# Kernel tuning notes

Hardware: AMD Instinct MI355X
Metric: run time of the kernel (lower is better)

The kernel has to match this reference:

```python
import math
import jax, jax.numpy as jnp
import numpy as np


def _scharr(img):
    # img: (..., H, W) -> (..., 2, H, W); F.conv2d is cross-correlation, as is lax.conv
    kx = jnp.array([[-3., 0., 3.], [10., 0., 10.], [-3., 0., 3.]], jnp.float32)
    k = jnp.stack([kx, kx.T])[:, None]  # (2,1,3,3)
    lead = img.shape[:-2]
    x = img.reshape((-1, 1) + img.shape[-2:])
    y = jax.lax.conv_general_dilated(x, k, (1, 1), 'SAME',
                                     dimension_numbers=('NCHW', 'OIHW', 'NCHW'))
    return y.reshape(lead + (2,) + img.shape[-2:])


def _rotate_nearest(x, angle_deg):
    # torchvision-style rotate with expand=True, nearest interpolation, zero fill
    H, W = x.shape[-2], x.shape[-1]
    a = math.radians(angle_deg)
    c, s = math.cos(a), math.sin(a)
    Hn = int(math.ceil(abs(W * s) + abs(H * c)))
    Wn = int(math.ceil(abs(W * c) + abs(H * s)))
    yy, xx = jnp.meshgrid(jnp.arange(Hn, dtype=jnp.float32),
                          jnp.arange(Wn, dtype=jnp.float32), indexing='ij')
    xg = xx - (Wn - 1) / 2.0
    yg = yy - (Hn - 1) / 2.0
    xi = c * xg - s * yg + (W - 1) / 2.0
    yi = s * xg + c * yg + (H - 1) / 2.0
    xn = jnp.round(xi).astype(jnp.int32)
    yn = jnp.round(yi).astype(jnp.int32)
    valid = (xn >= 0) & (xn < W) & (yn >= 0) & (yn < H)
    out = x[..., jnp.clip(yn, 0, H - 1), jnp.clip(xn, 0, W - 1)]
    return jnp.where(valid, out, jnp.zeros((), x.dtype))


def _gauss_derivs(img):
    # image_gaussian_derivatives: (B, C, H, W) -> (B, C, 8, H, W)
    H, W = img.shape[-2:]
    g = _scharr(img)  # (B, C, 2, H, W)
    # rotated_xywh(H, W, 45) to get crop offsets, exactly as in the source
    a = math.radians(45.0)
    al, be = math.cos(a), math.sin(a)
    cx, cy = W / 2.0, H / 2.0
    pts = [(0., 0.), (W - 1., 0.), (0., H - 1.), (W - 1., H - 1.)]
    rx = [al * px + be * py + (1 - al) * cx - be * cy for px, py in pts]
    ry = [-be * px + al * py + be * cx + (1 - al) * cy for px, py in pts]
    w45 = max(rx) - min(rx)
    h45 = max(ry) - min(ry)
    startx = int(max(0, (w45 - W) / 2))
    starty = int(max(0, (h45 - H) / 2))
    gr = _scharr(_rotate_nearest(img, 45.0))      # (B, C, 2, Hr, Wr)
    grb = _rotate_nearest(gr, -45.0)
    grc = grb[..., starty:starty + H, startx:startx + W]  # (B, C, 2, H, W)
    return jnp.concatenate([jnp.clip(g, 0, None), jnp.clip(g, None, 0),
                            jnp.clip(grc, 0, None), jnp.clip(grc, None, 0)], axis=-3)


def _normalize_min_max(x):
    hmin = x.min(axis=(-2, -1), keepdims=True)
    hmax = x.max(axis=(-2, -1), keepdims=True)
    return (x - hmin) / (hmax - hmin)


def _batched_hist(Z, nbins):
    # Z: (..., N) int in [0, nbins) -> per-row histogram (..., nbins) via one fused segment_sum
    lead = Z.shape[:-1]
    L = int(np.prod(lead))
    Zf = Z.reshape(L, -1)
    ids = (jnp.arange(L, dtype=jnp.int32)[:, None] * nbins + Zf).ravel()
    h = jax.ops.segment_sum(jnp.ones(ids.shape, jnp.float32), ids, num_segments=L * nbins)
    return h.reshape(lead + (nbins,))


def setup_inputs() -> dict:
    key = jax.random.key(0)
    k1, k2 = jax.random.split(key)
    img = jax.random.uniform(k1, (2, 3, 512, 512), jnp.float32)
    reg_lab = jax.random.randint(k2, (2, 1, 3, 512, 512), 0, 256, dtype=jnp.int32)
    return {'img': img, 'reg_lab': reg_lab,
            'color_bins': 25, 'texture_bins': 10, 'num_segments': 256}


def reference(img, reg_lab, color_bins, texture_bins, num_segments):
    B, I, G, H, W = reg_lab.shape
    C = img.shape[1]
    S = num_segments
    # normalized oriented gradient features (B, C, 8, H, W)
    tex = _normalize_min_max(_gauss_derivs(img))
    # region sizes: scatter_add of ones over region labels
    region_sizes = _batched_hist(reg_lab.reshape(B, I, G, H * W), S)  # (B,I,G,S)
    # color histograms
    Zc = (reg_lab[:, :, :, None].astype(jnp.float32) * color_bins
          + img[:, None, None] * (color_bins - 1)).astype(jnp.int32)  # (B,I,G,C,H,W)
    ch = _batched_hist(Zc.reshape(B, I, G, C, H * W), S * color_bins)
    ch = jnp.moveaxis(ch.reshape(B, I, G, C, S, color_bins), -2, -3)  # (B,I,G,S,C,cb)
    ch = ch / ch.sum(axis=(-2, -1), keepdims=True)
    # texture histograms
    Zt = (reg_lab[:, :, :, None, None].astype(jnp.float32) * texture_bins
          + tex[:, None, None] * (texture_bins - 1)).astype(jnp.int32)  # (B,I,G,C,8,H,W)
    th = _batched_hist(Zt.reshape(B, I, G, C, 8, H * W), S * texture_bins)
    th = jnp.moveaxis(th.reshape(B, I, G, C, 8, S, texture_bins), -2, -4)  # (B,I,G,S,C,8,tb)
    th = th / th.sum(axis=(-3, -2, -1), keepdims=True)
    # per-region bounding boxes via segment min/max (replaces the 5-deep python loop)
    grid_y, grid_x = jnp.meshgrid(jnp.arange(H, dtype=jnp.int32),
                                  jnp.arange(W, dtype=jnp.int32), indexing='ij')
    BIG = B * I * G
    ids = (jnp.arange(BIG, dtype=jnp.int32)[:, None] * S
           + reg_lab.reshape(BIG, H * W)).ravel()
    xs = jnp.tile(grid_x.ravel(), BIG)
    ys = jnp.tile(grid_y.ravel(), BIG)
    n = BIG * S
    xmin = jax.ops.segment_min(xs, ids, num_segments=n)
    xmax = jax.ops.segment_max(xs, ids, num_segments=n)
    ymin = jax.ops.segment_min(ys, ids, num_segments=n)
    ymax = jax.ops.segment_max(ys, ids, num_segments=n)
    nonempty = region_sizes.reshape(n) > 0
    xmin = jnp.where(nonempty, xmin, W)
    ymin = jnp.where(nonempty, ymin, H)
    xmax = jnp.where(nonempty, xmax, 0)
    ymax = jnp.where(nonempty, ymax, 0)
    xywh = jnp.stack([xmin, ymin, xmax - xmin, ymax - ymin], axis=-1).reshape(B, I, G, S, 4)
    return region_sizes, ch, th, xywh
```

## Files before the change

### kernel.cpp

```cpp
#include <hip/hip_runtime.h>
#include <climits>

#define HW 262144
#define IW 512
#define RN 725
#define NSEG 256
#define CH_OFF 1536
#define TH_OFF 116736
#define XY_OFF 485376
#define NBLK 256
#define THP 24
#define CHP 32

#define ASTR 67
#define RSTR 73
#define ROFF 156

static __device__ __forceinline__ float rtap_l(const float* __restrict__ Rt,
                                               int rx0, int ry0, int cx, int cy) {
    if (cx < 0 || cx >= RN || cy < 0 || cy >= RN) return 0.f;
    const float cs = 0.7071067811865476f;
    float xg = (float)cx - 362.0f;
    float yg = (float)cy - 362.0f;
    float xi = cs * xg - cs * yg + 255.5f;
    float yi = cs * xg + cs * yg + 255.5f;
    int xs = (int)rintf(xi);
    int ys = (int)rintf(yi);
    if (xs < 0 || xs >= IW || ys < 0 || ys >= IW) return 0.f;
    return Rt[(ys - ry0) * RSTR + (xs - rx0)];
}

static __device__ __forceinline__ void mm_of_map(const float* __restrict__ pmin,
                                                 const float* __restrict__ pmax,
                                                 int m, float* slo, float* shi,
                                                 float& mn, float& mx) {
    int tid = threadIdx.x;
    float lo = 3.4e38f, hi = -3.4e38f;
    for (int i = tid; i < NBLK; i += 256) {
        lo = fminf(lo, pmin[m * NBLK + i]);
        hi = fmaxf(hi, pmax[m * NBLK + i]);
    }
    slo[tid] = lo; shi[tid] = hi;
    __syncthreads();
    for (int off = 128; off > 0; off >>= 1) {
        if (tid < off) {
            slo[tid] = fminf(slo[tid], slo[tid + off]);
            shi[tid] = fmaxf(shi[tid], shi[tid + off]);
        }
        __syncthreads();
    }
    mn = slo[0]; mx = shi[0];
    __syncthreads();
}

__global__ __launch_bounds__(256) void k_grad(
    const float* __restrict__ img, const int* __restrict__ lab,
    float* __restrict__ gmaps,
    float* __restrict__ pmin, float* __restrict__ pmax,
    float* __restrict__ out, int* __restrict__ bbmin, int* __restrict__ bbmax,
    unsigned char* __restrict__ lab8)
{
    int t = blockIdx.x;
    int bc = blockIdx.y;
    int tid = threadIdx.x;
    if (bc == 0 && t < 6) {
        out[t * 256 + tid] = 0.0f;
    } else if (bc == 1 && t < 12) {
        int i = t * 256 + tid;
        bbmin[i] = INT_MAX;
        bbmax[i] = INT_MIN;
    }
    {
        int i = t * 256 + tid;
        int4 l = ((const int4*)(lab + (size_t)bc * HW))[i];
        unsigned v = (unsigned)(l.x & 255) | ((unsigned)(l.y & 255) << 8) |
                     ((unsigned)(l.z & 255) << 16) | ((unsigned)(l.w & 255) << 24);
        ((unsigned*)(lab8 + (size_t)bc * HW))[i] = v;
    }
    __shared__ float At[18 * ASTR];
    __shared__ float Rt[24 * RSTR];
    __shared__ float slo[4][256], shi[4][256];
    int tx0 = (t & 7) << 6;
    int ty0 = (t >> 3) << 4;
    const float* im = img + (size_t)bc * HW;
    int lane = tid & 63, wr = tid >> 6;
    for (int r = wr; r < 18; r += 4) {
        int gy = ty0 - 1 + r;
        bool yok = (gy >= 0 && gy < IW);
        int gx = tx0 - 1 + lane;
        At[r * ASTR + lane] = (yok && gx >= 0 && gx < IW) ? im[gy * IW + gx] : 0.f;
        if (lane < 2) {
            int gx2 = gx + 64;
            At[r * ASTR + lane + 64] = (yok && gx2 >= 0 && gx2 < IW) ? im[gy * IW + gx2] : 0.f;
        }
    }
    for (int r = wr; r < 24; r += 4) {
        int gy = ty0 - ROFF + r;
        bool yok = (gy >= 0 && gy < IW);
        int gx = tx0 - ROFF + lane;
        Rt[r * RSTR + lane] = (yok && gx >= 0 && gx < IW) ? im[gy * IW + gx] : 0.f;
        if (lane < 8) {
            int gx2 = gx + 64;
            Rt[r * RSTR + lane + 64] = (yok && gx2 >= 0 && gx2 < IW) ? im[gy * IW + gx2] : 0.f;
        }
    }
    __syncthreads();
    const float cs = 0.7071067811865476f;
    int rx0 = tx0 - ROFF, ry0 = ty0 - ROFF;
    float mn0 = 3.4e38f, mx0 = -3.4e38f, mn1 = 3.4e38f, mx1 = -3.4e38f;
    float mn2 = 3.4e38f, mx2 = -3.4e38f, mn3 = 3.4e38f, mx3 = -3.4e38f;
    #pragma unroll
    for (int it = 0; it < 4; ++it) {
        int ly = wr * 4 + it;
        int x = tx0 + lane, y = ty0 + ly;
        int p = y * IW + x;
        const float* Ar = At + ly * ASTR + lane;
        float a  = Ar[0],            b2 = Ar[1],            c2 = Ar[2];
        float d2 = Ar[ASTR],                                 e2 = Ar[ASTR + 2];
        float f2 = Ar[2 * ASTR],     h2 = Ar[2 * ASTR + 1], i9 = Ar[2 * ASTR + 2];
        float g0 = -3.f*a + 3.f*c2 + 10.f*d2 + 10.f*e2 - 3.f*f2 + 3.f*i9;
        float g1 = -3.f*a + 10.f*b2 - 3.f*c2 + 3.f*f2 + 10.f*h2 + 3.f*i9;
        gmaps[((size_t)(bc*2+0))*HW + p] = g0;
        gmaps[((size_t)(bc*2+1))*HW + p] = g1;
        float xgc = (float)(x + 105) - 512.5f;
        float ygc = (float)(y + 105) - 512.5f;
        float t1 = cs * xgc, t2 = cs * ygc;
        float xi = (t1 + t2) + 362.0f;
        float yi = (-t1 + t2) + 362.0f;
        int xn = (int)rintf(xi);
        int yn = (int)rintf(yi);
        float r0 = 0.f, r1 = 0.f;
        if (xn >= 0 && xn < RN && yn >= 0 && yn < RN) {
            float ra = rtap_l(Rt, rx0, ry0, xn-1, yn-1);
            float rb = rtap_l(Rt, rx0, ry0, xn,   yn-1);
            float rc = rtap_l(Rt, rx0, ry0, xn+1, yn-1);
            float rd = rtap_l(Rt, rx0, ry0, xn-1, yn);
            float re = rtap_l(Rt, rx0, ry0, xn+1, yn);
            float rf = rtap_l(Rt, rx0, ry0, xn-1, yn+1);
            float rh = rtap_l(Rt, rx0, ry0, xn,   yn+1);
            float ri = rtap_l(Rt, rx0, ry0, xn+1, yn+1);
            r0 = -3.f*ra + 3.f*rc + 10.f*rd + 10.f*re - 3.f*rf + 3.f*ri;
            r1 = -3.f*ra + 10.f*rb - 3.f*rc + 3.f*rf + 10.f*rh + 3.f*ri;
        }
        gmaps[((size_t)(12 + bc*2+0))*HW + p] = r0;
        gmaps[((size_t)(12 + bc*2+1))*HW + p] = r1;
        mn0 = fminf(mn0, g0); mx0 = fmaxf(mx0, g0);
        mn1 = fminf(mn1, g1); mx1 = fmaxf(mx1, g1);
        mn2 = fminf(mn2, r0); mx2 = fmaxf(mx2, r0);
        mn3 = fminf(mn3, r1); mx3 = fmaxf(mx3, r1);
    }
    slo[0][tid] = mn0; shi[0][tid] = mx0;
    slo[1][tid] = mn1; shi[1][tid] = mx1;
    slo[2][tid] = mn2; shi[2][tid] = mx2;
    slo[3][tid] = mn3; shi[3][tid] = mx3;
    __syncthreads();
    for (int off = 128; off > 0; off >>= 1) {
        if (tid < off) {
            #pragma unroll
            for (int k = 0; k < 4; ++k) {
                slo[k][tid] = fminf(slo[k][tid], slo[k][tid + off]);
                shi[k][tid] = fmaxf(shi[k][tid], shi[k][tid + off]);
            }
        }
        __syncthreads();
    }
    if (tid < 4) {
        int m = (tid < 2) ? (bc*2 + tid) : (12 + bc*2 + (tid - 2));
        pmin[m * NBLK + t] = slo[tid][0];
        pmax[m * NBLK + t] = shi[tid][0];
    }
}

__global__ __launch_bounds__(256) void k_regchist(
    const float* __restrict__ img, const unsigned char* __restrict__ lab8,
    float* __restrict__ rs_out, int* __restrict__ bbmin, int* __restrict__ bbmax,
    unsigned* __restrict__ chp)
{
    __shared__ unsigned cnt[NSEG * 25];
    __shared__ unsigned rcnt[NSEG];
    __shared__ int sxmin[NSEG], sxmax[NSEG], symin[NSEG], symax[NSEG];
    int gy = blockIdx.y;
    int c = gy % 3;
    int bg = gy / 3;
    int b = bg / 3;
    int tid = threadIdx.x;
    bool do_reg = (c == 0);
    for (int i = tid; i < NSEG * 25; i += 256) cnt[i] = 0;
    if (do_reg) {
        rcnt[tid] = 0; sxmin[tid] = INT_MAX; sxmax[tid] = INT_MIN;
        symin[tid] = INT_MAX; symax[tid] = INT_MIN;
    }
    __syncthreads();
    const float4* ip = (const float4*)(img + ((size_t)b * 3 + c) * HW);
    const unsigned* lp = (const unsigned*)(lab8 + (size_t)bg * HW);
    int stride = 256 * gridDim.x;
    for (int i = blockIdx.x * 256 + tid; i < HW / 4; i += stride) {
        float4 v4 = ip[i];
        unsigned l4 = lp[i];
        int l0 = l4 & 255, l1 = (l4 >> 8) & 255, l2 = (l4 >> 16) & 255, l3 = l4 >> 24;
        int b0 = (int)((float)l0 * 25.0f + v4.x * 24.0f);
        int b1 = (int)((float)l1 * 25.0f + v4.y * 24.0f);
        int b2 = (int)((float)l2 * 25.0f + v4.z * 24.0f);
        int b3 = (int)((float)l3 * 25.0f + v4.w * 24.0f);
        b0 = min(max(b0, 0), 6399); b1 = min(max(b1, 0), 6399);
        b2 = min(max(b2, 0), 6399); b3 = min(max(b3, 0), 6399);
        atomicAdd(&cnt[b0], 1u); atomicAdd(&cnt[b1], 1u);
        atomicAdd(&cnt[b2], 1u); atomicAdd(&cnt[b3], 1u);
        if (do_reg) {
            int p = i << 2;
            int y = p >> 9, x = p & 511;
            atomicAdd(&rcnt[l0], 1u); atomicAdd(&rcnt[l1], 1u);
            atomicAdd(&rcnt[l2], 1u); atomicAdd(&rcnt[l3], 1u);
            atomicMin(&sxmin[l0], x);     atomicMax(&sxmax[l0], x);
            atomicMin(&sxmin[l1], x + 1); atomicMax(&sxmax[l1], x + 1);
            atomicMin(&sxmin[l2], x + 2); atomicMax(&sxmax[l2], x + 2);
            atomicMin(&sxmin[l3], x + 3); atomicMax(&sxmax[l3], x + 3);
            atomicMin(&symin[l0], y); atomicMax(&symax[l0], y);
            atomicMin(&symin[l1], y); atomicMax(&symax[l1], y);
            atomicMin(&symin[l2], y); atomicMax(&symax[l2], y);
            atomicMin(&symin[l3], y); atomicMax(&symax[l3], y);
        }
    }
    __syncthreads();
    unsigned* dst = chp + ((size_t)gy * CHP + blockIdx.x) * 6400;
    for (int i = tid; i < NSEG * 25; i += 256) dst[i] = cnt[i];
    if (do_reg) {
        if (rcnt[tid]) atomicAdd(&rs_out[bg * NSEG + tid], (float)rcnt[tid]);
        if (sxmin[tid] != INT_MAX) {
            atomicMin(&bbmin[bg * NSEG + tid], sxmin[tid]);
            atomicMax(&bbmax[bg * NSEG + tid], sxmax[tid]);
            atomicMin(&bbmin[1536 + bg * NSEG + tid], symin[tid]);
            atomicMax(&bbmax[1536 + bg * NSEG + tid], symax[tid]);
        }
    }
}

__global__ __launch_bounds__(256) void k_thist(
    const float* __restrict__ maps, const unsigned char* __restrict__ lab8,
    const float* __restrict__ pmin, const float* __restrict__ pmax,
    unsigned* __restrict__ thp)
{
    __shared__ unsigned cnt[5120];
    __shared__ float slo[256], shi[256];
    int gy = blockIdx.y;
    int split = blockIdx.x;
    int gi = gy % 3;
    int r = gy / 3;
    int base = r & 1;
    int bd = r >> 1;
    int d = bd & 1;
    int bc = bd >> 1;
    int b = bc / 3;
    int m = base * 12 + bc * 2 + d;
    float mn, mx;
    mm_of_map(pmin, pmax, m, slo, shi, mn, mx);
    for (int i = threadIdx.x; i < 5120; i += 256) cnt[i] = 0;
    __syncthreads();
    float hminp = fmaxf(mn, 0.f), denp = fmaxf(mx, 0.f) - hminp;
    float hminn = fminf(mn, 0.f), denn = fminf(mx, 0.f) - hminn;
    const float4* src = (const float4*)(maps + (size_t)m * HW);
    const unsigned* lp = (const unsigned*)(lab8 + (size_t)(b * 3 + gi) * HW);
    for (int i = split * 256 + threadIdx.x; i < HW / 4; i += 256 * THP) {
        float4 v4 = src[i];
        unsigned l4 = lp[i];
#define TH1(V, SH)                                                     \
        {                                                              \
            float v = (V);                                             \
            bool ge = (v >= 0.f);                                      \
            float hm = ge ? hminp : hminn;                             \
            float dn = ge ? denp : denn;                               \
            float t9 = ((v - hm) / dn) * 9.0f;                         \
            int bi = (int)((float)((l4 >> SH) & 255u) * 10.0f + t9);   \
            bi = min(max(bi, 0), 2559);                                \
            atomicAdd(&cnt[(ge ? 0 : 2560) + bi], 1u);                 \
        }
        TH1(v4.x, 0) TH1(v4.y, 8) TH1(v4.z, 16) TH1(v4.w, 24)
#undef TH1
    }
    __syncthreads();
    unsigned* dst = thp + ((size_t)(gy * THP + split)) * 5120;
    for (int i = threadIdx.x; i < 5120; i += 256) dst[i] = cnt[i];
}

__global__ __launch_bounds__(256) void k_thfinal(
    const unsigned* __restrict__ thp, const unsigned* __restrict__ chp,
    const float* __restrict__ pmin, const float* __restrict__ pmax,
    const int* __restrict__ bbmin, const int* __restrict__ bbmax,
    float* __restrict__ out)
{
    int tid = threadIdx.x;
    int bx = blockIdx.x;
    if (bx < 288) {
        __shared__ unsigned hist[1280];
        __shared__ float slo[256], shi[256];
        int gy = bx >> 2;
        int ck = bx & 3;
        int l0 = ck << 6;
        int gi = gy % 3; int r = gy / 3; int base = r & 1;
        int bd = r >> 1; int d = bd & 1; int bc = bd >> 1;
        int b = bc / 3, c = bc - b * 3;
        int m = base * 12 + bc * 2 + d;
        float mn, mx;
        mm_of_map(pmin, pmax, m, slo, shi, mn, mx);
        int g0off = l0 * 10;
        for (int i = tid; i < 1280; i += 256) {
            int g = (i < 640) ? (g0off + i) : (2560 + g0off + (i - 640));
            unsigned s = 0;
            #pragma unroll 4
            for (int p = 0; p < THP; ++p) s += thp[((size_t)(gy * THP + p)) * 5120 + g];
            hist[i] = s;
        }
        __syncthreads();
        if (tid < 64) {
            int l = l0 + tid;
            unsigned nge = 0;
            for (int tb = 0; tb < 10; ++tb) nge += hist[tid * 10 + tb];
            float rsf = out[(b * 3 + gi) * NSEG + l];
            unsigned rsu = (unsigned)rsf;
            unsigned nlt = (rsu >= nge) ? (rsu - nge) : 0u;
            float hminp = fmaxf(mn, 0.f), denp = fmaxf(mx, 0.f) - hminp;
            float hminn = fminf(mn, 0.f), denn = fminf(mx, 0.f) - hminn;
            float la = (float)l;
            float tp0 = ((0.0f - hminp) / denp) * 9.0f;
            float tn0 = ((0.0f - hminn) / denn) * 9.0f;
            int bp = (int)(la * 10.0f + tp0); bp = min(max(bp, 0), 2559);
            int bn = (int)(la * 10.0f + tn0); bn = min(max(bn, 0), 2559);
            if (nlt && bp >= g0off && bp < g0off + 640) atomicAdd(&hist[bp - g0off], nlt);
            if (nge && bn >= g0off && bn < g0off + 640) atomicAdd(&hist[640 + bn - g0off], nge);
        }
        __syncthreads();
        for (int i = tid; i < 1280; i += 256) {
            int pos = (i < 640);
            int rr = pos ? i : i - 640;
            int seg = l0 + rr / 10, tb = rr % 10;
            int tt = base * 4 + (pos ? 0 : 2) + d;
            float rsf = out[(b * 3 + gi) * NSEG + seg];
            out[TH_OFF + ((size_t)((b * 3 + gi) * NSEG + seg) * 3 + c) * 80 + tt * 10 + tb] =
                (float)hist[i] / (24.0f * rsf);
        }
    } else {
        for (int seg = bx - 288; seg < 1536; seg += (gridDim.x - 288)) {
            int bg = seg >> 8;
            int s = seg & 255;
            float rsf = out[seg];
            float cd = 3.0f * rsf;
            float* ch = out + CH_OFF + (size_t)seg * 75;
            for (int i = tid; i < 75; i += 256) {
                int c = i / 25, cb = i - c * 25;
                unsigned sum = 0;
                const unsigned* src = chp + ((size_t)(bg * 3 + c) * CHP) * 6400 + s * 25 + cb;
                #pragma unroll 4
                for (int p = 0; p < CHP; ++p) sum += src[(size_t)p * 6400];
                ch[i] = (float)sum / cd;
            }
            if (tid == 0) {
                int xmin, xmax, ymin, ymax;
                if (rsf > 0.f) {
                    xmin = bbmin[seg]; ymin = bbmin[1536 + seg];
                    xmax = bbmax[seg]; ymax = bbmax[1536 + seg];
                } else {
                    xmin = IW; ymin = IW; xmax = 0; ymax = 0;
                }
                float* xy = out + XY_OFF + (size_t)seg * 4;
                xy[0] = (float)xmin; xy[1] = (float)ymin;
                xy[2] = (float)(xmax - xmin); xy[3] = (float)(ymax - ymin);
            }
        }
    }
}

extern "C" void kernel_launch(void* const* d_in, const int* in_sizes, int n_in,
                              void* d_out, int out_size, void* d_ws, size_t ws_size,
                              hipStream_t stream) {
    const float* img = (const float*)d_in[0];
    const int* lab = (const int*)d_in[1];
    float* out = (float*)d_out;

    float* gmaps = (float*)d_ws;
    float* pmin = gmaps + (size_t)24 * HW;
    float* pmax = pmin + 24 * NBLK;
    int* bbmin = (int*)(pmax + 24 * NBLK);
    int* bbmax = bbmin + 3072;
    unsigned* thp = (unsigned*)(bbmax + 3072);
    unsigned* chp = thp + (size_t)72 * THP * 5120;
    unsigned char* lab8 = (unsigned char*)(chp + (size_t)18 * CHP * 6400);

    hipLaunchKernelGGL(k_grad, dim3(NBLK, 6), dim3(256), 0, stream,
                       img, lab, gmaps, pmin, pmax, out, bbmin, bbmax, lab8);
    hipLaunchKernelGGL(k_regchist, dim3(CHP, 18), dim3(256), 0, stream,
                       img, lab8, out, bbmin, bbmax, chp);
    hipLaunchKernelGGL(k_thist, dim3(THP, 72), dim3(256), 0, stream, gmaps, lab8, pmin, pmax, thp);
    hipLaunchKernelGGL(k_thfinal, dim3(288 + 256), dim3(256), 0, stream, thp, chp, pmin, pmax, bbmin, bbmax, out);
}
```

Baseline: 131.8 us.

## Merge color and texture histogram kernels into one interleaved launch with packed 16-bit counters

Fuses k_regchist and k_thist into a single k_hist launch, giving every fourth block the color/region work and the other three the texture work, so the two histogram workloads run concurrently. The goal is to drop one launch and fill the GPU better. Color and region counts are now packed as two 16-bit counters per 32-bit word in shared memory, roughly halving the shared footprint to allow more resident blocks. The finalize kernel is widened to one block per segment instead of a strided loop. The packed counters risk overflow if a bin exceeds 65535 within a block's slice, but each slice holds only 8192 pixels, so they stay in range.

```diff
diff --git a/kernel.cpp b/kernel.cpp
--- a/kernel.cpp
+++ b/kernel.cpp
@@ -171,115 +171,128 @@
     }
 }
 
-__global__ __launch_bounds__(256) void k_regchist(
-    const float* __restrict__ img, const unsigned char* __restrict__ lab8,
-    float* __restrict__ rs_out, int* __restrict__ bbmin, int* __restrict__ bbmax,
-    unsigned* __restrict__ chp)
+__global__ __launch_bounds__(256) void k_hist(
+    const float* __restrict__ maps, const float* __restrict__ img,
+    const unsigned char* __restrict__ lab8,
+    const float* __restrict__ pmin, const float* __restrict__ pmax,
+    unsigned* __restrict__ thp, unsigned* __restrict__ chp,
+    float* __restrict__ rs_out, int* __restrict__ bbmin, int* __restrict__ bbmax)
 {
-    __shared__ unsigned cnt[NSEG * 25];
-    __shared__ unsigned rcnt[NSEG];
-    __shared__ int sxmin[NSEG], sxmax[NSEG], symin[NSEG], symax[NSEG];
-    int gy = blockIdx.y;
-    int c = gy % 3;
-    int bg = gy / 3;
-    int b = bg / 3;
+    __shared__ __align__(16) unsigned char smem[23040];
+    int bxid = blockIdx.x;
     int tid = threadIdx.x;
-    bool do_reg = (c == 0);
-    for (int i = tid; i < NSEG * 25; i += 256) cnt[i] = 0;
-    if (do_reg) {
-        rcnt[tid] = 0; sxmin[tid] = INT_MAX; sxmax[tid] = INT_MIN;
-        symin[tid] = INT_MAX; symax[tid] = INT_MIN;
-    }
-    __syncthreads();
-    const float4* ip = (const float4*)(img + ((size_t)b * 3 + c) * HW);
-    const unsigned* lp = (const unsigned*)(lab8 + (size_t)bg * HW);
-    int stride = 256 * gridDim.x;
-    for (int i = blockIdx.x * 256 + tid; i < HW / 4; i += stride) {
-        float4 v4 = ip[i];
-        unsigned l4 = lp[i];
-        int l0 = l4 & 255, l1 = (l4 >> 8) & 255, l2 = (l4 >> 16) & 255, l3 = l4 >> 24;
-        int b0 = (int)((float)l0 * 25.0f + v4.x * 24.0f);
-        int b1 = (int)((float)l1 * 25.0f + v4.y * 24.0f);
-        int b2 = (int)((float)l2 * 25.0f + v4.z * 24.0f);
-        int b3 = (int)((float)l3 * 25.0f + v4.w * 24.0f);
-        b0 = min(max(b0, 0), 6399); b1 = min(max(b1, 0), 6399);
-        b2 = min(max(b2, 0), 6399); b3 = min(max(b3, 0), 6399);
-        atomicAdd(&cnt[b0], 1u); atomicAdd(&cnt[b1], 1u);
-        atomicAdd(&cnt[b2], 1u); atomicAdd(&cnt[b3], 1u);
+    if ((bxid & 3) != 3) {
+        int idx = bxid - (bxid >> 2);
+        int gy = idx / THP;
+        int split = idx - gy * THP;
+        unsigned* cnt = (unsigned*)smem;
+        float* slo = (float*)(smem + 20480);
+        float* shi = slo + 256;
+        int gi = gy % 3;
+        int r = gy / 3;
+        int base = r & 1;
+        int bd = r >> 1;
+        int d = bd & 1;
+        int bc = bd >> 1;
+        int b = bc / 3;
+        int m = base * 12 + bc * 2 + d;
+        float mn, mx;
+        mm_of_map(pmin, pmax, m, slo, shi, mn, mx);
+        for (int i = tid; i < 5120; i += 256) cnt[i] = 0;
+        __syncthreads();
+        float hminp = fmaxf(mn, 0.f), denp = fmaxf(mx, 0.f) - hminp;
+        float hminn = fminf(mn, 0.f), denn = fminf(mx, 0.f) - hminn;
+        const float4* src = (const float4*)(maps + (size_t)m * HW);
+        const unsigned* lp = (const unsigned*)(lab8 + (size_t)(b * 3 + gi) * HW);
+        for (int i = split * 256 + tid; i < HW / 4; i += 256 * THP) {
+            float4 v4 = src[i];
+            unsigned l4 = lp[i];
+#define TH1(V, SH)                                                     \
+            {                                                          \
+                float v = (V);                                         \
+                bool ge = (v >= 0.f);                                  \
+                float hm = ge ? hminp : hminn;                         \
+                float dn = ge ? denp : denn;                           \
+                float t9 = ((v - hm) / dn) * 9.0f;                     \
+                int bi = (int)((float)((l4 >> SH) & 255u) * 10.0f + t9); \
+                bi = min(max(bi, 0), 2559);                            \
+                atomicAdd(&cnt[(ge ? 0 : 2560) + bi], 1u);             \
+            }
+            TH1(v4.x, 0) TH1(v4.y, 8) TH1(v4.z, 16) TH1(v4.w, 24)
+#undef TH1
+        }
+        __syncthreads();
+        unsigned* dst = thp + ((size_t)(gy * THP + split)) * 5120;
+        for (int i = tid; i < 5120; i += 256) dst[i] = cnt[i];
+    } else {
+        int w = bxid >> 2;
+        int gy = w >> 5;
+        int sp = w & 31;
+        int c = gy % 3;
+        int bg = gy / 3;
+        int b = bg / 3;
+        unsigned* pk = (unsigned*)smem;
+        unsigned* prc = pk + 3200;
+        int* sxmin = (int*)(prc + 128);
+        int* sxmax = sxmin + NSEG;
+        int* symin = sxmax + NSEG;
+        int* symax = symin + NSEG;
+        bool do_reg = (c == 0);
+        for (int i = tid; i < 3200; i += 256) pk[i] = 0;
         if (do_reg) {
-            int p = i << 2;
-            int y = p >> 9, x = p & 511;
-            atomicAdd(&rcnt[l0], 1u); atomicAdd(&rcnt[l1], 1u);
-            atomicAdd(&rcnt[l2], 1u); atomicAdd(&rcnt[l3], 1u);
-            atomicMin(&sxmin[l0], x);     atomicMax(&sxmax[l0], x);
-            atomicMin(&sxmin[l1], x + 1); atomicMax(&sxmax[l1], x + 1);
-            atomicMin(&sxmin[l2], x + 2); atomicMax(&sxmax[l2], x + 2);
-            atomicMin(&sxmin[l3], x + 3); atomicMax(&sxmax[l3], x + 3);
-            atomicMin(&symin[l0], y); atomicMax(&symax[l0], y);
-            atomicMin(&symin[l1], y); atomicMax(&symax[l1], y);
-            atomicMin(&symin[l2], y); atomicMax(&symax[l2], y);
-            atomicMin(&symin[l3], y); atomicMax(&symax[l3], y);
-        }
-    }
-    __syncthreads();
-    unsigned* dst = chp + ((size_t)gy * CHP + blockIdx.x) * 6400;
-    for (int i = tid; i < NSEG * 25; i += 256) dst[i] = cnt[i];
-    if (do_reg) {
-        if (rcnt[tid]) atomicAdd(&rs_out[bg * NSEG + tid], (float)rcnt[tid]);
-        if (sxmin[tid] != INT_MAX) {
-            atomicMin(&bbmin[bg * NSEG + tid], sxmin[tid]);
-            atomicMax(&bbmax[bg * NSEG + tid], sxmax[tid]);
-            atomicMin(&bbmin[1536 + bg * NSEG + tid], symin[tid]);
-            atomicMax(&bbmax[1536 + bg * NSEG + tid], symax[tid]);
-        }
-    }
-}
-
-__global__ __launch_bounds__(256) void k_thist(
-    const float* __restrict__ maps, const unsigned char* __restrict__ lab8,
-    const float* __restrict__ pmin, const float* __restrict__ pmax,
-    unsigned* __restrict__ thp)
-{
-    __shared__ unsigned cnt[5120];
-    __shared__ float slo[256], shi[256];
-    int gy = blockIdx.y;
-    int split = blockIdx.x;
-    int gi = gy % 3;
-    int r = gy / 3;
-    int base = r & 1;
-    int bd = r >> 1;
-    int d = bd & 1;
-    int bc = bd >> 1;
-    int b = bc / 3;
-    int m = base * 12 + bc * 2 + d;
-    float mn, mx;
-    mm_of_map(pmin, pmax, m, slo, shi, mn, mx);
-    for (int i = threadIdx.x; i < 5120; i += 256) cnt[i] = 0;
-    __syncthreads();
-    float hminp = fmaxf(mn, 0.f), denp = fmaxf(mx, 0.f) - hminp;
-    float hminn = fminf(mn, 0.f), denn = fminf(mx, 0.f) - hminn;
-    const float4* src = (const float4*)(maps + (size_t)m * HW);
-    const unsigned* lp = (const unsigned*)(lab8 + (size_t)(b * 3 + gi) * HW);
-    for (int i = split * 256 + threadIdx.x; i < HW / 4; i += 256 * THP) {
-        float4 v4 = src[i];
-        unsigned l4 = lp[i];
-#define TH1(V, SH)                                                     \
-        {                                                              \
-            float v = (V);                                             \
-            bool ge = (v >= 0.f);                                      \
-            float hm = ge ? hminp : hminn;                             \
-            float dn = ge ? denp : denn;                               \
-            float t9 = ((v - hm) / dn) * 9.0f;                         \
-            int bi = (int)((float)((l4 >> SH) & 255u) * 10.0f + t9);   \
-            bi = min(max(bi, 0), 2559);                                \
-            atomicAdd(&cnt[(ge ? 0 : 2560) + bi], 1u);                 \
-        }
-        TH1(v4.x, 0) TH1(v4.y, 8) TH1(v4.z, 16) TH1(v4.w, 24)
-#undef TH1
-    }
-    __syncthreads();
-    unsigned* dst = thp + ((size_t)(gy * THP + split)) * 5120;
-    for (int i = threadIdx.x; i < 5120; i += 256) dst[i] = cnt[i];
+            if (tid < 128) prc[tid] = 0;
+            sxmin[tid] = INT_MAX; sxmax[tid] = INT_MIN;
+            symin[tid] = INT_MAX; symax[tid] = INT_MIN;
+        }
+        __syncthreads();
+        const float4* ip = (const float4*)(img + ((size_t)b * 3 + c) * HW);
+        const unsigned* lp = (const unsigned*)(lab8 + (size_t)bg * HW);
+        for (int i = sp * 256 + tid; i < HW / 4; i += 256 * CHP) {
+            float4 v4 = ip[i];
+            unsigned l4 = lp[i];
+            int l0 = l4 & 255, l1 = (l4 >> 8) & 255, l2 = (l4 >> 16) & 255, l3 = l4 >> 24;
+            int b0 = (int)((float)l0 * 25.0f + v4.x * 24.0f);
+            int b1 = (int)((float)l1 * 25.0f + v4.y * 24.0f);
+            int b2 = (int)((float)l2 * 25.0f + v4.z * 24.0f);
+            int b3 = (int)((float)l3 * 25.0f + v4.w * 24.0f);
+            b0 = min(max(b0, 0), 6399); b1 = min(max(b1, 0), 6399);
+            b2 = min(max(b2, 0), 6399); b3 = min(max(b3, 0), 6399);
+            atomicAdd(&pk[b0 >> 1], 1u << ((b0 & 1) << 4));
+            atomicAdd(&pk[b1 >> 1], 1u << ((b1 & 1) << 4));
+            atomicAdd(&pk[b2 >> 1], 1u << ((b2 & 1) << 4));
+            atomicAdd(&pk[b3 >> 1], 1u << ((b3 & 1) << 4));
+            if (do_reg) {
+                int p = i << 2;
+                int y = p >> 9, x = p & 511;
+                atomicAdd(&prc[l0 >> 1], 1u << ((l0 & 1) << 4));
+                atomicAdd(&prc[l1 >> 1], 1u << ((l1 & 1) << 4));
+                atomicAdd(&prc[l2 >> 1], 1u << ((l2 & 1) << 4));
+                atomicAdd(&prc[l3 >> 1], 1u << ((l3 & 1) << 4));
+                atomicMin(&sxmin[l0], x);     atomicMax(&sxmax[l0], x);
+                atomicMin(&sxmin[l1], x + 1); atomicMax(&sxmax[l1], x + 1);
+                atomicMin(&sxmin[l2], x + 2); atomicMax(&sxmax[l2], x + 2);
+                atomicMin(&sxmin[l3], x + 3); atomicMax(&sxmax[l3], x + 3);
+                atomicMin(&symin[l0], y); atomicMax(&symax[l0], y);
+                atomicMin(&symin[l1], y); atomicMax(&symax[l1], y);
+                atomicMin(&symin[l2], y); atomicMax(&symax[l2], y);
+                atomicMin(&symin[l3], y); atomicMax(&symax[l3], y);
+            }
+        }
+        __syncthreads();
+        unsigned* dst = chp + ((size_t)gy * CHP + sp) * 6400;
+        for (int i = tid; i < 6400; i += 256)
+            dst[i] = (pk[i >> 1] >> ((i & 1) << 4)) & 0xFFFFu;
+        if (do_reg) {
+            unsigned rc = (prc[tid >> 1] >> ((tid & 1) << 4)) & 0xFFFFu;
+            if (rc) atomicAdd(&rs_out[bg * NSEG + tid], (float)rc);
+            if (sxmin[tid] != INT_MAX) {
+                atomicMin(&bbmin[bg * NSEG + tid], sxmin[tid]);
+                atomicMax(&bbmax[bg * NSEG + tid], sxmax[tid]);
+                atomicMin(&bbmin[1536 + bg * NSEG + tid], symin[tid]);
+                atomicMax(&bbmax[1536 + bg * NSEG + tid], symax[tid]);
+            }
+        }
+    }
 }
 
 __global__ __launch_bounds__(256) void k_thfinal(
@@ -332,39 +345,38 @@
         for (int i = tid; i < 1280; i += 256) {
             int pos = (i < 640);
             int rr = pos ? i : i - 640;
-            int seg = l0 + rr / 10, tb = rr % 10;
+            int lseg = rr / 10, tb = rr % 10;
+            int seg = l0 + lseg;
             int tt = base * 4 + (pos ? 0 : 2) + d;
             float rsf = out[(b * 3 + gi) * NSEG + seg];
             out[TH_OFF + ((size_t)((b * 3 + gi) * NSEG + seg) * 3 + c) * 80 + tt * 10 + tb] =
                 (float)hist[i] / (24.0f * rsf);
         }
     } else {
-        for (int seg = bx - 288; seg < 1536; seg += (gridDim.x - 288)) {
-            int bg = seg >> 8;
-            int s = seg & 255;
-            float rsf = out[seg];
-            float cd = 3.0f * rsf;
-            float* ch = out + CH_OFF + (size_t)seg * 75;
-            for (int i = tid; i < 75; i += 256) {
-                int c = i / 25, cb = i - c * 25;
-                unsigned sum = 0;
-                const unsigned* src = chp + ((size_t)(bg * 3 + c) * CHP) * 6400 + s * 25 + cb;
-                #pragma unroll 4
-                for (int p = 0; p < CHP; ++p) sum += src[(size_t)p * 6400];
-                ch[i] = (float)sum / cd;
+        int seg = bx - 288;
+        int bg = seg >> 8;
+        int s = seg & 255;
+        float rsf = out[seg];
+        float cd = 3.0f * rsf;
+        float* ch = out + CH_OFF + (size_t)seg * 75;
+        if (tid < 75) {
+            int c = tid / 25, cb = tid - c * 25;
+            unsigned sum = 0;
+            const unsigned* src = chp + ((size_t)(bg * 3 + c) * CHP) * 6400 + s * 25 + cb;
+            #pragma unroll 4
+            for (int p = 0; p < CHP; ++p) sum += src[(size_t)p * 6400];
+            ch[tid] = (float)sum / cd;
+        } else if (tid == 75) {
+            int xmin, xmax, ymin, ymax;
+            if (rsf > 0.f) {
+                xmin = bbmin[seg]; ymin = bbmin[1536 + seg];
+                xmax = bbmax[seg]; ymax = bbmax[1536 + seg];
+            } else {
+                xmin = IW; ymin = IW; xmax = 0; ymax = 0;
             }
-            if (tid == 0) {
-                int xmin, xmax, ymin, ymax;
-                if (rsf > 0.f) {
-                    xmin = bbmin[seg]; ymin = bbmin[1536 + seg];
-                    xmax = bbmax[seg]; ymax = bbmax[1536 + seg];
-                } else {
-                    xmin = IW; ymin = IW; xmax = 0; ymax = 0;
-                }
-                float* xy = out + XY_OFF + (size_t)seg * 4;
-                xy[0] = (float)xmin; xy[1] = (float)ymin;
-                xy[2] = (float)(xmax - xmin); xy[3] = (float)(ymax - ymin);
-            }
+            float* xy = out + XY_OFF + (size_t)seg * 4;
+            xy[0] = (float)xmin; xy[1] = (float)ymin;
+            xy[2] = (float)(xmax - xmin); xy[3] = (float)(ymax - ymin);
         }
     }
 }
@@ -387,8 +399,8 @@
 
     hipLaunchKernelGGL(k_grad, dim3(NBLK, 6), dim3(256), 0, stream,
                        img, lab, gmaps, pmin, pmax, out, bbmin, bbmax, lab8);
-    hipLaunchKernelGGL(k_regchist, dim3(CHP, 18), dim3(256), 0, stream,
-                       img, lab8, out, bbmin, bbmax, chp);
-    hipLaunchKernelGGL(k_thist, dim3(THP, 72), dim3(256), 0, stream, gmaps, lab8, pmin, pmax, thp);
-    hipLaunchKernelGGL(k_thfinal, dim3(288 + 256), dim3(256), 0, stream, thp, chp, pmin, pmax, bbmin, bbmax, out);
-}
+    hipLaunchKernelGGL(k_hist, dim3(2304), dim3(256), 0, stream,
+                       gmaps, img, lab8, pmin, pmax, thp, chp, out, bbmin, bbmax);
+    hipLaunchKernelGGL(k_thfinal, dim3(288 + 1536), dim3(256), 0, stream,
+                       thp, chp, pmin, pmax, bbmin, bbmax, out);
+}
```

Result: faster. 125.7 us (-4.6%).
